# Kernel tuning notes

Hardware: AMD Instinct MI355X
Metric: run time of the kernel (lower is better)

Reference implementation:

```python
import jax, jax.numpy as jnp
import numpy as np

TAU = 2.0
V_TH = 1.0
V_RESET = 0.0
ALPHA = 2.0  # ATan surrogate alpha (spikingjelly default)

@jax.custom_vjp
def spike(x):
    # Heaviside forward, ATan surrogate backward
    return (x >= 0).astype(x.dtype)

def _spike_fwd(x):
    return spike(x), x

def _spike_bwd(x, g):
    pix = (jnp.pi / 2) * ALPHA * x
    return (g * (ALPHA / 2) / (1 + pix * pix),)

spike.defvjp(_spike_fwd, _spike_bwd)

def setup_inputs() -> dict:
    key = jax.random.key(0)
    k1, k2, k3 = jax.random.split(key, 3)
    T, B, I, H = 256, 128, 512, 512
    x = jax.random.normal(k1, (T, B, I), dtype=jnp.float32)
    W = jax.random.normal(k2, (H, I), dtype=jnp.float32) * (1.0 / np.sqrt(I))
    b = jax.random.normal(k3, (H,), dtype=jnp.float32) * 0.01
    return {"x": x, "W": W, "b": b}

def reference(x, W, b):
    # Linear projection over all timesteps at once: (T,B,I) @ (H,I)^T -> (T,B,H)
    h = jnp.einsum('tbi,hi->tbh', x, W) + b

    def step(v, ht):
        # LIFNode, decay_input=False, v_reset=0: charge, fire, hard reset
        v = v - (v - V_RESET) / TAU + ht
        s = spike(v - V_TH)
        s_d = jax.lax.stop_gradient(s)  # detach_reset=True
        v = v * (1.0 - s_d) + V_RESET * s_d
        return v, s

    v0 = jnp.zeros_like(h[0])
    _, spikes = jax.lax.scan(step, v0, h)
    # dropout_p=0 (inference) -> identity; no synapse filter
    return spikes
```

## Files before the change

### kernel.cpp

```cpp
#include <hip/hip_runtime.h>

#define T_STEPS 256
#define B_DIM   128
#define I_DIM   512
#define H_DIM   512
#define M_DIM   (T_STEPS * B_DIM)

#define BM 128
#define BN 128
#define BK 32

__global__ __launch_bounds__(256, 3) void gemm_bias_f32(
    const float* __restrict__ A,
    const float* __restrict__ Bw,
    const float* __restrict__ bias,
    float* __restrict__ C)
{
    __shared__ float As[BK * BM];
    __shared__ float Bs[BK * BN];

    const int tid = threadIdx.x;
    const int tx  = tid & 15;
    const int ty  = tid >> 4;
    const int m0  = blockIdx.y * BM;
    const int n0  = blockIdx.x * BN;

    float acc[8][8];
    #pragma unroll
    for (int i = 0; i < 8; i++)
        #pragma unroll
        for (int j = 0; j < 8; j++)
            acc[i][j] = 0.0f;

    const int lrow = tid >> 3;
    const int lk   = (tid & 7) * 4;
    const int q    = tid & 7;

    const float* Aptr = A  + (size_t)(m0 + lrow) * I_DIM + lk;
    const float* Bptr = Bw + (size_t)(n0 + lrow) * I_DIM + lk;

    for (int k0 = 0; k0 < I_DIM; k0 += BK) {
        float4 av[4], bv[4];
        #pragma unroll
        for (int p = 0; p < 4; p++) {
            av[p] = *(const float4*)(Aptr + (size_t)(p * 32) * I_DIM + k0);
            bv[p] = *(const float4*)(Bptr + (size_t)(p * 32) * I_DIM + k0);
        }

        __syncthreads();

        #pragma unroll
        for (int p = 0; p < 4; p++) {
            const int r    = lrow + p * 32;
            const int base = (((r >> 2) ^ q) << 2) + (r & 3);
            As[(lk + 0) * BM + base] = av[p].x;
            As[(lk + 1) * BM + base] = av[p].y;
            As[(lk + 2) * BM + base] = av[p].z;
            As[(lk + 3) * BM + base] = av[p].w;
            Bs[(lk + 0) * BN + base] = bv[p].x;
            Bs[(lk + 1) * BN + base] = bv[p].y;
            Bs[(lk + 2) * BN + base] = bv[p].z;
            Bs[(lk + 3) * BN + base] = bv[p].w;
        }

        __syncthreads();

        const float4* As4 = (const float4*)As;
        const float4* Bs4 = (const float4*)Bs;
        for (int k = 0; k < BK; k++) {
            const int rho = (k >> 2) & 7;
            float4 a0 = As4[k * (BM / 4) + ((ty * 2)     ^ rho)];
            float4 a1 = As4[k * (BM / 4) + ((ty * 2 + 1) ^ rho)];
            float4 b0 = Bs4[k * (BN / 4) + (tx        ^ rho)];
            float4 b1 = Bs4[k * (BN / 4) + ((16 + tx) ^ rho)];
            float a[8] = {a0.x, a0.y, a0.z, a0.w, a1.x, a1.y, a1.z, a1.w};
            float b[8] = {b0.x, b0.y, b0.z, b0.w, b1.x, b1.y, b1.z, b1.w};
            #pragma unroll
            for (int i = 0; i < 8; i++)
                #pragma unroll
                for (int j = 0; j < 8; j++)
                    acc[i][j] = fmaf(a[i], b[j], acc[i][j]);
        }
    }

    float4 bc0 = *(const float4*)(bias + n0 + tx * 4);
    float4 bc1 = *(const float4*)(bias + n0 + 64 + tx * 4);

    #pragma unroll
    for (int i = 0; i < 8; i++) {
        const int m = m0 + ty * 8 + i;
        float4 o0, o1;
        o0.x = acc[i][0] + bc0.x;
        o0.y = acc[i][1] + bc0.y;
        o0.z = acc[i][2] + bc0.z;
        o0.w = acc[i][3] + bc0.w;
        o1.x = acc[i][4] + bc1.x;
        o1.y = acc[i][5] + bc1.y;
        o1.z = acc[i][6] + bc1.z;
        o1.w = acc[i][7] + bc1.w;
        float* cp = C + (size_t)m * H_DIM + n0;
        *(float4*)(cp + tx * 4)      = o0;
        *(float4*)(cp + 64 + tx * 4) = o1;
    }
}

#define SCAN_U 32
__global__ __launch_bounds__(256) void lif_scan(
    const float* __restrict__ h,
    float* __restrict__ out)
{
    const int n   = B_DIM * H_DIM;
    const int idx = blockIdx.x * 256 + threadIdx.x;
    const float* hp = h + idx;
    float* op = out + idx;

    float bufA[SCAN_U], bufB[SCAN_U];

    #pragma unroll
    for (int i = 0; i < SCAN_U; i++)
        bufA[i] = hp[(size_t)i * n];

    float v = 0.0f;
    for (int t0 = 0; t0 < T_STEPS; t0 += 2 * SCAN_U) {
        #pragma unroll
        for (int i = 0; i < SCAN_U; i++)
            bufB[i] = hp[(size_t)(t0 + SCAN_U + i) * n];

        #pragma unroll
        for (int i = 0; i < SCAN_U; i++) {
            v = fmaf(0.5f, v, bufA[i]);
            const bool fire = (v >= 1.0f);
            __builtin_nontemporal_store(fire ? 1.0f : 0.0f,
                                        op + (size_t)(t0 + i) * n);
            v = fire ? 0.0f : v;
        }

        if (t0 + 2 * SCAN_U < T_STEPS) {
            #pragma unroll
            for (int i = 0; i < SCAN_U; i++)
                bufA[i] = hp[(size_t)(t0 + 2 * SCAN_U + i) * n];
        }

        #pragma unroll
        for (int i = 0; i < SCAN_U; i++) {
            v = fmaf(0.5f, v, bufB[i]);
            const bool fire = (v >= 1.0f);
            __builtin_nontemporal_store(fire ? 1.0f : 0.0f,
                                        op + (size_t)(t0 + SCAN_U + i) * n);
            v = fire ? 0.0f : v;
        }
    }
}

extern "C" void kernel_launch(void* const* d_in, const int* in_sizes, int n_in,
                              void* d_out, int out_size, void* d_ws, size_t ws_size,
                              hipStream_t stream) {
    const float* x = (const float*)d_in[0];
    const float* W = (const float*)d_in[1];
    const float* b = (const float*)d_in[2];
    float* out = (float*)d_out;
    float* h   = (float*)d_ws;

    dim3 grid(H_DIM / BN, M_DIM / BM);
    gemm_bias_f32<<<grid, 256, 0, stream>>>(x, W, b, h);

    lif_scan<<<(B_DIM * H_DIM) / 256, 256, 0, stream>>>(h, out);
}
```

Measured before the change: 321.1 us.

## Fuse GEMM and LIF scan into one kernel tiled over time per batch

Replaces the separate GEMM and LIF-scan kernels with one kernel. Each block owns one batch row and 128 hidden units, computes 128-timestep GEMM tiles, stages the biased results in shared memory, and runs the sequential LIF recurrence from there. This avoids writing and re-reading the full intermediate h tensor in global memory and drops one launch. The cost is that the scan runs on only half the threads while the other threads idle, A-tile loads are strided by B*I per row, and occupancy is lower (launch bounds 2, larger shared memory).

Result: faster. 300.8 us (-6.3%).

```diff
diff --git a/kernel.cpp b/kernel.cpp
--- a/kernel.cpp
+++ b/kernel.cpp
@@ -4,150 +4,125 @@
 #define B_DIM   128
 #define I_DIM   512
 #define H_DIM   512
-#define M_DIM   (T_STEPS * B_DIM)
 
-#define BM 128
-#define BN 128
 #define BK 32
 
-__global__ __launch_bounds__(256, 3) void gemm_bias_f32(
+__global__ __launch_bounds__(256, 2) void fused_gemm_lif(
     const float* __restrict__ A,
     const float* __restrict__ Bw,
     const float* __restrict__ bias,
-    float* __restrict__ C)
+    float* __restrict__ out)
 {
-    __shared__ float As[BK * BM];
-    __shared__ float Bs[BK * BN];
+    __shared__ float smem[128 * 132];
+    float* Asm = smem;
+    float* Bsm = smem + BK * 128;
 
     const int tid = threadIdx.x;
     const int tx  = tid & 15;
     const int ty  = tid >> 4;
-    const int m0  = blockIdx.y * BM;
-    const int n0  = blockIdx.x * BN;
-
-    float acc[8][8];
-    #pragma unroll
-    for (int i = 0; i < 8; i++)
-        #pragma unroll
-        for (int j = 0; j < 8; j++)
-            acc[i][j] = 0.0f;
+    const int n0  = blockIdx.x * 128;
+    const int b   = blockIdx.y;
 
     const int lrow = tid >> 3;
     const int lk   = (tid & 7) * 4;
     const int q    = tid & 7;
 
-    const float* Aptr = A  + (size_t)(m0 + lrow) * I_DIM + lk;
     const float* Bptr = Bw + (size_t)(n0 + lrow) * I_DIM + lk;
 
-    for (int k0 = 0; k0 < I_DIM; k0 += BK) {
-        float4 av[4], bv[4];
+    const float4 bc0 = *(const float4*)(bias + n0 + tx * 4);
+    const float4 bc1 = *(const float4*)(bias + n0 + 64 + tx * 4);
+
+    float v = 0.0f;
+
+    for (int t0 = 0; t0 < T_STEPS; t0 += 128) {
+        float acc[8][8];
         #pragma unroll
-        for (int p = 0; p < 4; p++) {
-            av[p] = *(const float4*)(Aptr + (size_t)(p * 32) * I_DIM + k0);
-            bv[p] = *(const float4*)(Bptr + (size_t)(p * 32) * I_DIM + k0);
+        for (int i = 0; i < 8; i++)
+            #pragma unroll
+            for (int j = 0; j < 8; j++)
+                acc[i][j] = 0.0f;
+
+        for (int k0 = 0; k0 < I_DIM; k0 += BK) {
+            float4 av[4], bv[4];
+            #pragma unroll
+            for (int p = 0; p < 4; p++) {
+                const int t = t0 + lrow + p * 32;
+                av[p] = *(const float4*)(A + ((size_t)t * B_DIM + b) * I_DIM
+                                           + lk + k0);
+                bv[p] = *(const float4*)(Bptr + (size_t)(p * 32) * I_DIM + k0);
+            }
+
+            __syncthreads();
+
+            #pragma unroll
+            for (int p = 0; p < 4; p++) {
+                const int r    = lrow + p * 32;
+                const int base = (((r >> 2) ^ q) << 2) | (r & 3);
+                Asm[(lk + 0) * 128 + base] = av[p].x;
+                Asm[(lk + 1) * 128 + base] = av[p].y;
+                Asm[(lk + 2) * 128 + base] = av[p].z;
+                Asm[(lk + 3) * 128 + base] = av[p].w;
+                Bsm[(lk + 0) * 128 + base] = bv[p].x;
+                Bsm[(lk + 1) * 128 + base] = bv[p].y;
+                Bsm[(lk + 2) * 128 + base] = bv[p].z;
+                Bsm[(lk + 3) * 128 + base] = bv[p].w;
+            }
+
+            __syncthreads();
+
+            const float4* As4 = (const float4*)Asm;
+            const float4* Bs4 = (const float4*)Bsm;
+            for (int k = 0; k < BK; k++) {
+                const int rho = (k >> 2) & 7;
+                float4 a0 = As4[k * 32 + ((ty * 2)     ^ rho)];
+                float4 a1 = As4[k * 32 + ((ty * 2 + 1) ^ rho)];
+                float4 b0 = Bs4[k * 32 + (tx        ^ rho)];
+                float4 b1 = Bs4[k * 32 + ((16 + tx) ^ rho)];
+                float a[8] = {a0.x, a0.y, a0.z, a0.w, a1.x, a1.y, a1.z, a1.w};
+                float bb[8] = {b0.x, b0.y, b0.z, b0.w, b1.x, b1.y, b1.z, b1.w};
+                #pragma unroll
+                for (int i = 0; i < 8; i++)
+                    #pragma unroll
+                    for (int j = 0; j < 8; j++)
+                        acc[i][j] = fmaf(a[i], bb[j], acc[i][j]);
+            }
         }
 
         __syncthreads();
 
         #pragma unroll
-        for (int p = 0; p < 4; p++) {
-            const int r    = lrow + p * 32;
-            const int base = (((r >> 2) ^ q) << 2) + (r & 3);
-            As[(lk + 0) * BM + base] = av[p].x;
-            As[(lk + 1) * BM + base] = av[p].y;
-            As[(lk + 2) * BM + base] = av[p].z;
-            As[(lk + 3) * BM + base] = av[p].w;
-            Bs[(lk + 0) * BN + base] = bv[p].x;
-            Bs[(lk + 1) * BN + base] = bv[p].y;
-            Bs[(lk + 2) * BN + base] = bv[p].z;
-            Bs[(lk + 3) * BN + base] = bv[p].w;
+        for (int i = 0; i < 8; i++) {
+            float* hp = smem + (ty * 8 + i) * 132;
+            float4 o0, o1;
+            o0.x = acc[i][0] + bc0.x;
+            o0.y = acc[i][1] + bc0.y;
+            o0.z = acc[i][2] + bc0.z;
+            o0.w = acc[i][3] + bc0.w;
+            o1.x = acc[i][4] + bc1.x;
+            o1.y = acc[i][5] + bc1.y;
+            o1.z = acc[i][6] + bc1.z;
+            o1.w = acc[i][7] + bc1.w;
+            *(float4*)(hp + tx * 4)      = o0;
+            *(float4*)(hp + 64 + tx * 4) = o1;
         }
 
         __syncthreads();
 
-        const float4* As4 = (const float4*)As;
-        const float4* Bs4 = (const float4*)Bs;
-        for (int k = 0; k < BK; k++) {
-            const int rho = (k >> 2) & 7;
-            float4 a0 = As4[k * (BM / 4) + ((ty * 2)     ^ rho)];
-            float4 a1 = As4[k * (BM / 4) + ((ty * 2 + 1) ^ rho)];
-            float4 b0 = Bs4[k * (BN / 4) + (tx        ^ rho)];
-            float4 b1 = Bs4[k * (BN / 4) + ((16 + tx) ^ rho)];
-            float a[8] = {a0.x, a0.y, a0.z, a0.w, a1.x, a1.y, a1.z, a1.w};
-            float b[8] = {b0.x, b0.y, b0.z, b0.w, b1.x, b1.y, b1.z, b1.w};
-            #pragma unroll
-            for (int i = 0; i < 8; i++)
+        if (tid < 128) {
+            for (int tb = 0; tb < 128; tb += 8) {
+                float hv[8];
                 #pragma unroll
-                for (int j = 0; j < 8; j++)
-                    acc[i][j] = fmaf(a[i], b[j], acc[i][j]);
-        }
-    }
-
-    float4 bc0 = *(const float4*)(bias + n0 + tx * 4);
-    float4 bc1 = *(const float4*)(bias + n0 + 64 + tx * 4);
-
-    #pragma unroll
-    for (int i = 0; i < 8; i++) {
-        const int m = m0 + ty * 8 + i;
-        float4 o0, o1;
-        o0.x = acc[i][0] + bc0.x;
-        o0.y = acc[i][1] + bc0.y;
-        o0.z = acc[i][2] + bc0.z;
-        o0.w = acc[i][3] + bc0.w;
-        o1.x = acc[i][4] + bc1.x;
-        o1.y = acc[i][5] + bc1.y;
-        o1.z = acc[i][6] + bc1.z;
-        o1.w = acc[i][7] + bc1.w;
-        float* cp = C + (size_t)m * H_DIM + n0;
-        *(float4*)(cp + tx * 4)      = o0;
-        *(float4*)(cp + 64 + tx * 4) = o1;
-    }
-}
-
-#define SCAN_U 32
-__global__ __launch_bounds__(256) void lif_scan(
-    const float* __restrict__ h,
-    float* __restrict__ out)
-{
-    const int n   = B_DIM * H_DIM;
-    const int idx = blockIdx.x * 256 + threadIdx.x;
-    const float* hp = h + idx;
-    float* op = out + idx;
-
-    float bufA[SCAN_U], bufB[SCAN_U];
-
-    #pragma unroll
-    for (int i = 0; i < SCAN_U; i++)
-        bufA[i] = hp[(size_t)i * n];
-
-    float v = 0.0f;
-    for (int t0 = 0; t0 < T_STEPS; t0 += 2 * SCAN_U) {
-        #pragma unroll
-        for (int i = 0; i < SCAN_U; i++)
-            bufB[i] = hp[(size_t)(t0 + SCAN_U + i) * n];
-
-        #pragma unroll
-        for (int i = 0; i < SCAN_U; i++) {
-            v = fmaf(0.5f, v, bufA[i]);
-            const bool fire = (v >= 1.0f);
-            __builtin_nontemporal_store(fire ? 1.0f : 0.0f,
-                                        op + (size_t)(t0 + i) * n);
-            v = fire ? 0.0f : v;
-        }
-
-        if (t0 + 2 * SCAN_U < T_STEPS) {
-            #pragma unroll
-            for (int i = 0; i < SCAN_U; i++)
-                bufA[i] = hp[(size_t)(t0 + 2 * SCAN_U + i) * n];
-        }
-
-        #pragma unroll
-        for (int i = 0; i < SCAN_U; i++) {
-            v = fmaf(0.5f, v, bufB[i]);
-            const bool fire = (v >= 1.0f);
-            __builtin_nontemporal_store(fire ? 1.0f : 0.0f,
-                                        op + (size_t)(t0 + SCAN_U + i) * n);
-            v = fire ? 0.0f : v;
+                for (int i = 0; i < 8; i++)
+                    hv[i] = smem[(tb + i) * 132 + tid];
+                #pragma unroll
+                for (int i = 0; i < 8; i++) {
+                    v = 0.5f * v + hv[i];
+                    const bool fire = (v >= 1.0f);
+                    out[((size_t)(t0 + tb + i) * B_DIM + b) * H_DIM + n0 + tid]
+                        = fire ? 1.0f : 0.0f;
+                    v = fire ? 0.0f : v;
+                }
+            }
         }
     }
 }
@@ -159,10 +134,8 @@
     const float* W = (const float*)d_in[1];
     const float* b = (const float*)d_in[2];
     float* out = (float*)d_out;
-    float* h   = (float*)d_ws;
+    (void)d_ws; (void)ws_size;
 
-    dim3 grid(H_DIM / BN, M_DIM / BM);
-    gemm_bias_f32<<<grid, 256, 0, stream>>>(x, W, b, h);
-
-    lif_scan<<<(B_DIM * H_DIM) / 256, 256, 0, stream>>>(h, out);
+    dim3 grid(H_DIM / 128, B_DIM);
+    fused_gemm_lif<<<grid, 256, 0, stream>>>(x, W, b, out);
 }
```
